# Kernel tuning notes

Measured on AMD Instinct MI355X. Metric: run time of the kernel, lower is better.

## Reference

```python
import jax, jax.numpy as jnp
import numpy as np

N_EPS_ROWS = 8194   # 1 center + 8192 eps + 1 noise
D_IN = 2048
D_OUT = 2048
NW = 4096
NB = 2048


def setup_inputs() -> dict:
    key = jax.random.key(0)
    ks = jax.random.split(key, 8)
    return {
        "x": jax.random.normal(ks[0], (N_EPS_ROWS, D_IN), jnp.float32),
        "x_true": jax.random.normal(ks[1], (32, D_IN), jnp.float32),
        "W": jax.random.normal(ks[2], (D_OUT, D_IN), jnp.float32) * 0.02,
        "b": jax.random.normal(ks[3], (D_OUT,), jnp.float32) * 0.02,
        "w_val": jax.random.normal(ks[4], (NW,), jnp.float32) * 0.01,
        "b_val": jax.random.normal(ks[5], (NB,), jnp.float32) * 0.01,
        "w_idx": jax.random.randint(ks[6], (NW,), 0, D_OUT * D_IN, jnp.int64 if jax.config.jax_enable_x64 else jnp.int32),
        "b_idx": jax.random.randint(ks[7], (NB,), 0, D_OUT, jnp.int64 if jax.config.jax_enable_x64 else jnp.int32),
    }


def reference(x, x_true, W, b, w_val, b_val, w_idx, b_idx):
    # x: [K, D_in] with row 0 = center, rows 1:-1 = eps terms, row -1 = noise
    d_out, d_in = W.shape
    x_center = x[0]                                   # [D_in]
    x_true_out = x_true @ W.T + b                     # [B, D_out]
    x_value = x[0] @ W.T + b                          # [D_out]
    x_eps = x[1:-1] @ W.T                             # [E, D_out] (bias zeroed)
    x_noise = x[-1] @ jnp.abs(W).T                    # [D_out] (|W|, bias zeroed)

    # One-hot weight perturbation: W_eps has single entry v at flat index idx.
    # Forward of center through it = v * x_center[idx % d_in] at out-row idx // d_in.
    rows_w = w_idx // d_in
    cols_w = w_idx % d_in
    nw = w_idx.shape[0]
    add_w = jnp.zeros((nw, d_out), x.dtype).at[jnp.arange(nw), rows_w].set(
        w_val * x_center[cols_w])

    # One-hot bias perturbation applied to zero input: output is the one-hot bias.
    nb = b_idx.shape[0]
    add_b = jnp.zeros((nb, d_out), x.dtype).at[jnp.arange(nb), b_idx].set(b_val)

    # Order matches torch code: weight-eps rows inserted before noise, then bias-eps.
    x_out = jnp.concatenate(
        [x_value[None], x_eps, add_w, add_b, x_noise[None]], axis=0)
    abs_sum = jnp.sum(jnp.abs(x_out[1:]), axis=0)
    x_min = x_out[0] - abs_sum
    x_max = x_out[0] + abs_sum
    return (x_out, x_min, x_max, x_true_out)
```

## Files before the change

kernel.cpp:

```cpp
#include <hip/hip_runtime.h>


typedef __bf16 bf16_t;
typedef bf16_t bf16x8 __attribute__((ext_vector_type(8)));
typedef float f32x4 __attribute__((ext_vector_type(4)));

#define D 2048
#define NKT 32
#define ROW_ADDW 8193
#define ROW_ADDB 12289
#define ROW_NOISE 14337
#define N_OUT_ROWS 14338
#define OUT_MIN ((size_t)N_OUT_ROWS * D)
#define OUT_MAX (OUT_MIN + D)
#define OUT_XTRUE (OUT_MAX + D)

#define GLOAD_LDS16(g, l)                                                 \
  __builtin_amdgcn_global_load_lds(                                       \
      (__attribute__((address_space(1))) void*)(g),                       \
      (__attribute__((address_space(3))) void*)(l), 16, 0, 0)

#define LDSF(base, row, c2)                                               \
  (*(const bf16x8*)((const char*)(base) + (row) * 128 + ((c2) ^ (((row) & 7) << 4))))

__global__ __launch_bounds__(256) void convert_eps(const float* __restrict__ x,
                                                   bf16_t* __restrict__ Xb) {
  const int row = blockIdx.x;
  const int c = threadIdx.x * 8;
  const float* src = x + (size_t)(row + 1) * D + c;
  float4 f0 = *(const float4*)(src);
  float4 f1 = *(const float4*)(src + 4);
  bf16x8 o;
  o[0] = (bf16_t)f0.x; o[1] = (bf16_t)f0.y; o[2] = (bf16_t)f0.z; o[3] = (bf16_t)f0.w;
  o[4] = (bf16_t)f1.x; o[5] = (bf16_t)f1.y; o[6] = (bf16_t)f1.z; o[7] = (bf16_t)f1.w;
  *(bf16x8*)(Xb + (size_t)row * D + c) = o;
}

__global__ __launch_bounds__(256) void convert_w(const float* __restrict__ W,
                                                 bf16_t* __restrict__ Wb) {
  const int row = blockIdx.x;
  const int c = threadIdx.x * 8;
  const float* src = W + (size_t)row * D + c;
  float4 f0 = *(const float4*)(src);
  float4 f1 = *(const float4*)(src + 4);
  bf16x8 o;
  o[0] = (bf16_t)f0.x; o[1] = (bf16_t)f0.y; o[2] = (bf16_t)f0.z; o[3] = (bf16_t)f0.w;
  o[4] = (bf16_t)f1.x; o[5] = (bf16_t)f1.y; o[6] = (bf16_t)f1.z; o[7] = (bf16_t)f1.w;
  *(bf16x8*)(Wb + (size_t)row * D + c) = o;
}

__global__ __launch_bounds__(512, 2) void gemm8_kernel(const bf16_t* __restrict__ Xb,
                                                       const bf16_t* __restrict__ Wb,
                                                       float* __restrict__ out,
                                                       float* __restrict__ gpart) {
  __shared__ bf16_t lds[65536];
  const int tid = threadIdx.x;
  const int wid = tid >> 6, l = tid & 63;
  const int wm = wid >> 2, wn = wid & 3;
  const int g4 = l >> 4, r16 = l & 15;
  const int mt = blockIdx.y, nt = blockIdx.x;
  const int m0 = mt * 256, n0 = nt * 256;
  const int sr = tid >> 3;
  const int scol = ((tid & 7) ^ (sr & 7)) << 3;

  f32x4 acc[8][4] = {};

#define STAGE_HALF(G, row0, k0, ldsoff)                                          \
  {                                                                              \
    const bf16_t* _s0 = (G) + (size_t)((row0) + sr) * D + (k0) + scol;           \
    const bf16_t* _s1 = (G) + (size_t)((row0) + 64 + sr) * D + (k0) + scol;      \
    GLOAD_LDS16(_s0, &lds[(ldsoff) + tid * 8]);                                  \
    GLOAD_LDS16(_s1, &lds[(ldsoff) + 4096 + tid * 8]);                           \
  }

  STAGE_HALF(Xb, m0, 0, 0);
  STAGE_HALF(Xb, m0 + 128, 0, 8192);
  STAGE_HALF(Wb, n0, 0, 16384);
  STAGE_HALF(Wb, n0 + 128, 0, 24576);
  STAGE_HALF(Wb, n0, 64, 32768 + 16384);
  STAGE_HALF(Wb, n0 + 128, 64, 32768 + 24576);
  asm volatile("s_waitcnt vmcnt(4)" ::: "memory");
  __builtin_amdgcn_sched_barrier(0);
  __builtin_amdgcn_s_barrier();
  __builtin_amdgcn_sched_barrier(0);

  for (int t = 0; t < NKT; ++t) {
    const int bufA = (t & 1) << 15;
    const int bufN = ((t + 1) & 1) << 15;
    const int k1 = (((t + 1) & (NKT - 1)) << 6);
    const int k2 = (((t + 2) & (NKT - 1)) << 6);
    const bf16_t* Areg = &lds[bufA];
    const bf16_t* Breg = &lds[bufA + 16384];

    bf16x8 b[4][2];
    bf16x8 a[2][2];

#pragma unroll
    for (int q = 0; q < 4; ++q) {
      if (q == 0) {
#pragma unroll
        for (int n = 0; n < 4; ++n)
#pragma unroll
          for (int kk = 0; kk < 2; ++kk)
            b[n][kk] = LDSF(Breg, wn * 64 + n * 16 + r16, kk * 64 + g4 * 16);
      }
#pragma unroll
      for (int f = 0; f < 2; ++f)
#pragma unroll
        for (int kk = 0; kk < 2; ++kk)
          a[f][kk] = LDSF(Areg, wm * 128 + q * 32 + f * 16 + r16, kk * 64 + g4 * 16);
      if (q == 0)      STAGE_HALF(Xb, m0,       k1, bufN)
      else if (q == 1) STAGE_HALF(Xb, m0 + 128, k1, bufN + 8192)
      else if (q == 2) STAGE_HALF(Wb, n0,       k2, bufA + 16384)
      else             STAGE_HALF(Wb, n0 + 128, k2, bufA + 24576)
      __builtin_amdgcn_sched_barrier(0);
      __builtin_amdgcn_s_barrier();
      __builtin_amdgcn_sched_barrier(0);
      __builtin_amdgcn_s_setprio(1);
#pragma unroll
      for (int f = 0; f < 2; ++f)
#pragma unroll
        for (int n = 0; n < 4; ++n)
#pragma unroll
          for (int kk = 0; kk < 2; ++kk)
            acc[q * 2 + f][n] = __builtin_amdgcn_mfma_f32_16x16x32_bf16(
                a[f][kk], b[n][kk], acc[q * 2 + f][n], 0, 0, 0);
      __builtin_amdgcn_s_setprio(0);
      __builtin_amdgcn_sched_barrier(0);
      if (q == 3) {
        asm volatile("s_waitcnt vmcnt(4)" ::: "memory");
        __builtin_amdgcn_sched_barrier(0);
      }
      __builtin_amdgcn_s_barrier();
      __builtin_amdgcn_sched_barrier(0);
    }
  }

#pragma unroll
  for (int m = 0; m < 8; ++m) {
    const int grow = m0 + wm * 128 + m * 16 + g4 * 4;
#pragma unroll
    for (int n = 0; n < 4; ++n) {
      const int gc = n0 + wn * 64 + n * 16 + r16;
#pragma unroll
      for (int j = 0; j < 4; ++j)
        out[(size_t)(grow + j + 1) * D + gc] = acc[m][n][j];
    }
  }
#pragma unroll
  for (int n = 0; n < 4; ++n) {
    float s = 0.f;
#pragma unroll
    for (int m = 0; m < 8; ++m)
#pragma unroll
      for (int j = 0; j < 4; ++j)
        s += fabsf(acc[m][n][j]);
    s += __shfl_xor(s, 16, 64);
    s += __shfl_xor(s, 32, 64);
    if (g4 == 0)
      gpart[(size_t)(mt * 2 + wm) * D + n0 + wn * 64 + n * 16 + r16] = s;
  }
#undef STAGE_HALF
}

__global__ __launch_bounds__(256) void smallrows_partial(const float* __restrict__ x,
                                                         const float* __restrict__ x_true,
                                                         const float* __restrict__ W,
                                                         float* __restrict__ spart) {
  const int j = blockIdx.x * 256 + threadIdx.x;
  const int kb = blockIdx.y;
  const float* wrow = W + (size_t)j * D + kb * 64;
  const float* xc = x + kb * 64;
  const float* xn = x + (size_t)8193 * D + kb * 64;
  const float* xt = x_true + kb * 64;
  float acc[34];
#pragma unroll
  for (int r = 0; r < 34; ++r) acc[r] = 0.f;
  for (int k = 0; k < 64; k += 4) {
    float4 w = *(const float4*)(wrow + k);
    float4 v = *(const float4*)(xc + k);
    acc[0] += w.x * v.x + w.y * v.y + w.z * v.z + w.w * v.w;
#pragma unroll
    for (int r = 0; r < 32; ++r) {
      float4 u = *(const float4*)(xt + (size_t)r * D + k);
      acc[1 + r] += w.x * u.x + w.y * u.y + w.z * u.z + w.w * u.w;
    }
    float4 nn = *(const float4*)(xn + k);
    acc[33] += fabsf(w.x) * nn.x + fabsf(w.y) * nn.y + fabsf(w.z) * nn.z + fabsf(w.w) * nn.w;
  }
#pragma unroll
  for (int r = 0; r < 34; ++r)
    spart[((size_t)kb * 34 + r) * D + j] = acc[r];
}

__global__ __launch_bounds__(256) void smallrows_final(const float* __restrict__ spart,
                                                       const float* __restrict__ bias,
                                                       float* __restrict__ out) {
  const int j = blockIdx.x * 256 + threadIdx.x;
  const int r = blockIdx.y;
  float s = 0.f;
#pragma unroll 8
  for (int kb = 0; kb < 32; ++kb) s += spart[((size_t)kb * 34 + r) * D + j];
  if (r == 0)       out[j] = s + bias[j];
  else if (r <= 32) out[OUT_XTRUE + (size_t)(r - 1) * D + j] = s + bias[j];
  else              out[(size_t)ROW_NOISE * D + j] = s;
}

__global__ __launch_bounds__(256) void scatter_kernel(const float* __restrict__ x,
                                                      const float* __restrict__ w_val,
                                                      const float* __restrict__ b_val,
                                                      const int* __restrict__ w_idx,
                                                      const int* __restrict__ b_idx,
                                                      float* __restrict__ out,
                                                      float* __restrict__ absacc) {
  const int i = blockIdx.x * 256 + threadIdx.x;
  if (i < 4096) {
    const int idx = w_idx[i];
    const int row = idx / D, col = idx % D;
    const float v = w_val[i] * x[col];
    out[(size_t)(ROW_ADDW + i) * D + row] = v;
    atomicAdd(&absacc[row], fabsf(v));
  }
  const int ib = i - 4096;
  if (ib >= 0 && ib < 2048) {
    const float v = b_val[ib];
    out[(size_t)(ROW_ADDB + ib) * D + b_idx[ib]] = v;
    atomicAdd(&absacc[b_idx[ib]], fabsf(v));
  }
}

__global__ __launch_bounds__(256) void final_minmax(const float* __restrict__ gpart,
                                                    const float* __restrict__ absacc,
                                                    float* __restrict__ out) {
  const int col = blockIdx.x * 256 + threadIdx.x;
  float s = absacc[col];
#pragma unroll 8
  for (int p = 0; p < 64; ++p) s += gpart[(size_t)p * D + col];
  s += fabsf(out[(size_t)ROW_NOISE * D + col]);
  const float c = out[col];
  out[OUT_MIN + col] = c - s;
  out[OUT_MAX + col] = c + s;
}

extern "C" void kernel_launch(void* const* d_in, const int* in_sizes, int n_in,
                              void* d_out, int out_size, void* d_ws, size_t ws_size,
                              hipStream_t stream) {
  const float* x      = (const float*)d_in[0];
  const float* x_true = (const float*)d_in[1];
  const float* W      = (const float*)d_in[2];
  const float* b      = (const float*)d_in[3];
  const float* w_val  = (const float*)d_in[4];
  const float* b_val  = (const float*)d_in[5];
  const int*   w_idx  = (const int*)d_in[6];
  const int*   b_idx  = (const int*)d_in[7];
  float* out = (float*)d_out;

  char* ws = (char*)d_ws;
  bf16_t* Xb    = (bf16_t*)ws;
  bf16_t* Wb    = (bf16_t*)(ws + 33554432);
  float*  gpart = (float*)(ws + 41943040);
  float*  spart = (float*)(ws + 42467328);
  float*  absacc= (float*)(ws + 51380224);

  hipMemsetAsync(out + (size_t)ROW_ADDW * D, 0, (size_t)6144 * D * sizeof(float), stream);
  hipMemsetAsync(absacc, 0, D * sizeof(float), stream);

  convert_eps<<<dim3(8192), 256, 0, stream>>>(x, Xb);
  convert_w<<<dim3(D), 256, 0, stream>>>(W, Wb);
  gemm8_kernel<<<dim3(8, 32), 512, 0, stream>>>(Xb, Wb, out, gpart);
  smallrows_partial<<<dim3(8, 32), 256, 0, stream>>>(x, x_true, W, spart);
  smallrows_final<<<dim3(8, 34), 256, 0, stream>>>(spart, b, out);
  scatter_kernel<<<dim3(24), 256, 0, stream>>>(x, w_val, b_val, w_idx, b_idx, out, absacc);
  final_minmax<<<dim3(8), 256, 0, stream>>>(gpart, absacc, out);
}
```

Before: 305.7 us.

## Fuse conversion and small-row kernels, remap GEMM tiles, restructure MFMA k-loop

Merges the two bf16 conversion kernels into one launch that also zeroes the abs-sum accumulator row, replacing a memset. Replaces the two-pass split-K small-row GEMV with one wave-per-output kernel using shuffle reductions, fused with the scatter kernel. The GEMM gets a block-index remap for L2 locality, drops the occupancy hint from launch bounds, and reorders the inner loop over k-halves with fewer live fragment registers, staging both W halves in the last quarter. This cuts launch count and intermediate traffic but changes pipeline timing and register pressure in the main GEMM.

```diff
diff --git a/kernel.cpp b/kernel.cpp
--- a/kernel.cpp
+++ b/kernel.cpp
@@ -23,42 +23,47 @@
 #define LDSF(base, row, c2)                                               \
   (*(const bf16x8*)((const char*)(base) + (row) * 128 + ((c2) ^ (((row) & 7) << 4))))
 
-__global__ __launch_bounds__(256) void convert_eps(const float* __restrict__ x,
-                                                   bf16_t* __restrict__ Xb) {
-  const int row = blockIdx.x;
+__global__ __launch_bounds__(256) void convert_all(const float* __restrict__ x,
+                                                   const float* __restrict__ W,
+                                                   bf16_t* __restrict__ Xb,
+                                                   bf16_t* __restrict__ Wb,
+                                                   float* __restrict__ gpart) {
+  const int bid = blockIdx.x;
   const int c = threadIdx.x * 8;
-  const float* src = x + (size_t)(row + 1) * D + c;
+  if (bid == 10240) {
+    *(float4*)(gpart + 64 * D + c) = float4{0.f, 0.f, 0.f, 0.f};
+    *(float4*)(gpart + 64 * D + c + 4) = float4{0.f, 0.f, 0.f, 0.f};
+    return;
+  }
+  const float* src;
+  bf16_t* dst;
+  if (bid < 8192) {
+    src = x + (size_t)(bid + 1) * D + c;
+    dst = Xb + (size_t)bid * D + c;
+  } else {
+    src = W + (size_t)(bid - 8192) * D + c;
+    dst = Wb + (size_t)(bid - 8192) * D + c;
+  }
   float4 f0 = *(const float4*)(src);
   float4 f1 = *(const float4*)(src + 4);
   bf16x8 o;
   o[0] = (bf16_t)f0.x; o[1] = (bf16_t)f0.y; o[2] = (bf16_t)f0.z; o[3] = (bf16_t)f0.w;
   o[4] = (bf16_t)f1.x; o[5] = (bf16_t)f1.y; o[6] = (bf16_t)f1.z; o[7] = (bf16_t)f1.w;
-  *(bf16x8*)(Xb + (size_t)row * D + c) = o;
-}
-
-__global__ __launch_bounds__(256) void convert_w(const float* __restrict__ W,
-                                                 bf16_t* __restrict__ Wb) {
-  const int row = blockIdx.x;
-  const int c = threadIdx.x * 8;
-  const float* src = W + (size_t)row * D + c;
-  float4 f0 = *(const float4*)(src);
-  float4 f1 = *(const float4*)(src + 4);
-  bf16x8 o;
-  o[0] = (bf16_t)f0.x; o[1] = (bf16_t)f0.y; o[2] = (bf16_t)f0.z; o[3] = (bf16_t)f0.w;
-  o[4] = (bf16_t)f1.x; o[5] = (bf16_t)f1.y; o[6] = (bf16_t)f1.z; o[7] = (bf16_t)f1.w;
-  *(bf16x8*)(Wb + (size_t)row * D + c) = o;
-}
-
-__global__ __launch_bounds__(512, 2) void gemm8_kernel(const bf16_t* __restrict__ Xb,
-                                                       const bf16_t* __restrict__ Wb,
-                                                       float* __restrict__ out,
-                                                       float* __restrict__ gpart) {
+  *(bf16x8*)dst = o;
+}
+
+__global__ __launch_bounds__(512) void gemm8_kernel(const bf16_t* __restrict__ Xb,
+                                                    const bf16_t* __restrict__ Wb,
+                                                    float* __restrict__ out,
+                                                    float* __restrict__ gpart) {
   __shared__ bf16_t lds[65536];
   const int tid = threadIdx.x;
   const int wid = tid >> 6, l = tid & 63;
   const int wm = wid >> 2, wn = wid & 3;
   const int g4 = l >> 4, r16 = l & 15;
-  const int mt = blockIdx.y, nt = blockIdx.x;
+  const int f = blockIdx.y * 8 + blockIdx.x;
+  const int orig = (f & 7) * 32 + (f >> 3);
+  const int mt = orig >> 3, nt = orig & 7;
   const int m0 = mt * 256, n0 = nt * 256;
   const int sr = tid >> 3;
   const int scol = ((tid & 7) ^ (sr & 7)) << 3;
@@ -92,39 +97,37 @@
     const bf16_t* Areg = &lds[bufA];
     const bf16_t* Breg = &lds[bufA + 16384];
 
-    bf16x8 b[4][2];
-    bf16x8 a[2][2];
+    bf16x8 bb[4];
+    bf16x8 a[4];
 
 #pragma unroll
     for (int q = 0; q < 4; ++q) {
-      if (q == 0) {
+      const int kk = q >> 1;
+      const int mh = (q & 1) * 4;
+      if ((q & 1) == 0) {
 #pragma unroll
         for (int n = 0; n < 4; ++n)
-#pragma unroll
-          for (int kk = 0; kk < 2; ++kk)
-            b[n][kk] = LDSF(Breg, wn * 64 + n * 16 + r16, kk * 64 + g4 * 16);
-      }
-#pragma unroll
-      for (int f = 0; f < 2; ++f)
-#pragma unroll
-        for (int kk = 0; kk < 2; ++kk)
-          a[f][kk] = LDSF(Areg, wm * 128 + q * 32 + f * 16 + r16, kk * 64 + g4 * 16);
+          bb[n] = LDSF(Breg, wn * 64 + n * 16 + r16, kk * 64 + g4 * 16);
+      }
+#pragma unroll
+      for (int m = 0; m < 4; ++m)
+        a[m] = LDSF(Areg, wm * 128 + (mh + m) * 16 + r16, kk * 64 + g4 * 16);
       if (q == 0)      STAGE_HALF(Xb, m0,       k1, bufN)
       else if (q == 1) STAGE_HALF(Xb, m0 + 128, k1, bufN + 8192)
-      else if (q == 2) STAGE_HALF(Wb, n0,       k2, bufA + 16384)
-      else             STAGE_HALF(Wb, n0 + 128, k2, bufA + 24576)
+      else if (q == 3) {
+        STAGE_HALF(Wb, n0,       k2, bufA + 16384)
+        STAGE_HALF(Wb, n0 + 128, k2, bufA + 24576)
+      }
       __builtin_amdgcn_sched_barrier(0);
       __builtin_amdgcn_s_barrier();
       __builtin_amdgcn_sched_barrier(0);
       __builtin_amdgcn_s_setprio(1);
 #pragma unroll
-      for (int f = 0; f < 2; ++f)
+      for (int m = 0; m < 4; ++m)
 #pragma unroll
         for (int n = 0; n < 4; ++n)
-#pragma unroll
-          for (int kk = 0; kk < 2; ++kk)
-            acc[q * 2 + f][n] = __builtin_amdgcn_mfma_f32_16x16x32_bf16(
-                a[f][kk], b[n][kk], acc[q * 2 + f][n], 0, 0, 0);
+          acc[mh + m][n] = __builtin_amdgcn_mfma_f32_16x16x32_bf16(
+              a[m], bb[n], acc[mh + m][n], 0, 0, 0);
       __builtin_amdgcn_s_setprio(0);
       __builtin_amdgcn_sched_barrier(0);
       if (q == 3) {
@@ -163,79 +166,77 @@
 #undef STAGE_HALF
 }
 
-__global__ __launch_bounds__(256) void smallrows_partial(const float* __restrict__ x,
-                                                         const float* __restrict__ x_true,
-                                                         const float* __restrict__ W,
-                                                         float* __restrict__ spart) {
-  const int j = blockIdx.x * 256 + threadIdx.x;
-  const int kb = blockIdx.y;
-  const float* wrow = W + (size_t)j * D + kb * 64;
-  const float* xc = x + kb * 64;
-  const float* xn = x + (size_t)8193 * D + kb * 64;
-  const float* xt = x_true + kb * 64;
-  float acc[34];
-#pragma unroll
-  for (int r = 0; r < 34; ++r) acc[r] = 0.f;
-  for (int k = 0; k < 64; k += 4) {
-    float4 w = *(const float4*)(wrow + k);
-    float4 v = *(const float4*)(xc + k);
-    acc[0] += w.x * v.x + w.y * v.y + w.z * v.z + w.w * v.w;
-#pragma unroll
-    for (int r = 0; r < 32; ++r) {
-      float4 u = *(const float4*)(xt + (size_t)r * D + k);
-      acc[1 + r] += w.x * u.x + w.y * u.y + w.z * u.z + w.w * u.w;
-    }
-    float4 nn = *(const float4*)(xn + k);
-    acc[33] += fabsf(w.x) * nn.x + fabsf(w.y) * nn.y + fabsf(w.z) * nn.z + fabsf(w.w) * nn.w;
-  }
-#pragma unroll
-  for (int r = 0; r < 34; ++r)
-    spart[((size_t)kb * 34 + r) * D + j] = acc[r];
-}
-
-__global__ __launch_bounds__(256) void smallrows_final(const float* __restrict__ spart,
-                                                       const float* __restrict__ bias,
-                                                       float* __restrict__ out) {
-  const int j = blockIdx.x * 256 + threadIdx.x;
-  const int r = blockIdx.y;
-  float s = 0.f;
-#pragma unroll 8
-  for (int kb = 0; kb < 32; ++kb) s += spart[((size_t)kb * 34 + r) * D + j];
-  if (r == 0)       out[j] = s + bias[j];
-  else if (r <= 32) out[OUT_XTRUE + (size_t)(r - 1) * D + j] = s + bias[j];
-  else              out[(size_t)ROW_NOISE * D + j] = s;
-}
-
-__global__ __launch_bounds__(256) void scatter_kernel(const float* __restrict__ x,
-                                                      const float* __restrict__ w_val,
-                                                      const float* __restrict__ b_val,
-                                                      const int* __restrict__ w_idx,
-                                                      const int* __restrict__ b_idx,
-                                                      float* __restrict__ out,
-                                                      float* __restrict__ absacc) {
-  const int i = blockIdx.x * 256 + threadIdx.x;
+__global__ __launch_bounds__(256) void small_scatter(const float* __restrict__ x,
+                                                     const float* __restrict__ x_true,
+                                                     const float* __restrict__ W,
+                                                     const float* __restrict__ bias,
+                                                     const float* __restrict__ w_val,
+                                                     const float* __restrict__ b_val,
+                                                     const int* __restrict__ w_idx,
+                                                     const int* __restrict__ b_idx,
+                                                     float* __restrict__ out,
+                                                     float* __restrict__ gpart) {
+  const int bid = blockIdx.x;
+  const int tid = threadIdx.x;
+  if (bid < 512) {
+    const int w = tid >> 6, l = tid & 63;
+    const int j = bid * 4 + w;
+    const float* wrow = W + (size_t)j * D;
+    const float* xn = x + (size_t)8193 * D;
+    float accc = 0.f, accn = 0.f;
+    float acct[32] = {};
+    for (int it = 0; it < 8; ++it) {
+      const int k = it * 256 + l * 4;
+      float4 w4 = *(const float4*)(wrow + k);
+      float4 c4 = *(const float4*)(x + k);
+      accc += w4.x * c4.x + w4.y * c4.y + w4.z * c4.z + w4.w * c4.w;
+      float4 n4 = *(const float4*)(xn + k);
+      accn += fabsf(w4.x) * n4.x + fabsf(w4.y) * n4.y + fabsf(w4.z) * n4.z + fabsf(w4.w) * n4.w;
+#pragma unroll
+      for (int r = 0; r < 32; ++r) {
+        float4 t4 = *(const float4*)(x_true + (size_t)r * D + k);
+        acct[r] += w4.x * t4.x + w4.y * t4.y + w4.z * t4.z + w4.w * t4.w;
+      }
+    }
+#pragma unroll
+    for (int off = 32; off; off >>= 1) {
+      accc += __shfl_xor(accc, off, 64);
+      accn += __shfl_xor(accn, off, 64);
+#pragma unroll
+      for (int r = 0; r < 32; ++r) acct[r] += __shfl_xor(acct[r], off, 64);
+    }
+    if (l == 0) {
+      const float bj = bias[j];
+      out[j] = accc + bj;
+      out[(size_t)ROW_NOISE * D + j] = accn;
+#pragma unroll
+      for (int r = 0; r < 32; ++r)
+        out[OUT_XTRUE + (size_t)r * D + j] = acct[r] + bj;
+    }
+    return;
+  }
+  const int i = (bid - 512) * 256 + tid;
   if (i < 4096) {
     const int idx = w_idx[i];
-    const int row = idx / D, col = idx % D;
+    const int row = idx >> 11, col = idx & 2047;
     const float v = w_val[i] * x[col];
     out[(size_t)(ROW_ADDW + i) * D + row] = v;
-    atomicAdd(&absacc[row], fabsf(v));
+    atomicAdd(&gpart[64 * D + row], fabsf(v));
   }
   const int ib = i - 4096;
   if (ib >= 0 && ib < 2048) {
     const float v = b_val[ib];
     out[(size_t)(ROW_ADDB + ib) * D + b_idx[ib]] = v;
-    atomicAdd(&absacc[b_idx[ib]], fabsf(v));
+    atomicAdd(&gpart[64 * D + b_idx[ib]], fabsf(v));
   }
 }
 
 __global__ __launch_bounds__(256) void final_minmax(const float* __restrict__ gpart,
-                                                    const float* __restrict__ absacc,
                                                     float* __restrict__ out) {
   const int col = blockIdx.x * 256 + threadIdx.x;
-  float s = absacc[col];
-#pragma unroll 8
-  for (int p = 0; p < 64; ++p) s += gpart[(size_t)p * D + col];
+  float s = 0.f;
+#pragma unroll 5
+  for (int p = 0; p < 65; ++p) s += gpart[(size_t)p * D + col];
   s += fabsf(out[(size_t)ROW_NOISE * D + col]);
   const float c = out[col];
   out[OUT_MIN + col] = c - s;
@@ -259,17 +260,11 @@
   bf16_t* Xb    = (bf16_t*)ws;
   bf16_t* Wb    = (bf16_t*)(ws + 33554432);
   float*  gpart = (float*)(ws + 41943040);
-  float*  spart = (float*)(ws + 42467328);
-  float*  absacc= (float*)(ws + 51380224);
 
   hipMemsetAsync(out + (size_t)ROW_ADDW * D, 0, (size_t)6144 * D * sizeof(float), stream);
-  hipMemsetAsync(absacc, 0, D * sizeof(float), stream);
-
-  convert_eps<<<dim3(8192), 256, 0, stream>>>(x, Xb);
-  convert_w<<<dim3(D), 256, 0, stream>>>(W, Wb);
+  convert_all<<<dim3(10241), 256, 0, stream>>>(x, W, Xb, Wb, gpart);
   gemm8_kernel<<<dim3(8, 32), 512, 0, stream>>>(Xb, Wb, out, gpart);
-  smallrows_partial<<<dim3(8, 32), 256, 0, stream>>>(x, x_true, W, spart);
-  smallrows_final<<<dim3(8, 34), 256, 0, stream>>>(spart, b, out);
-  scatter_kernel<<<dim3(24), 256, 0, stream>>>(x, w_val, b_val, w_idx, b_idx, out, absacc);
-  final_minmax<<<dim3(8), 256, 0, stream>>>(gpart, absacc, out);
-}
+  small_scatter<<<dim3(536), 256, 0, stream>>>(x, x_true, W, b, w_val, b_val,
+                                               w_idx, b_idx, out, gpart);
+  final_minmax<<<dim3(8), 256, 0, stream>>>(gpart, out);
+}
```

Result: slower. 332.0 us (+8.6%).
